# Optimization experiments

Measured on AMD Instinct MI355X. Metric: run time of the kernel, lower is better.

Reference implementation:

```python
import jax, jax.numpy as jnp
import numpy as np

NUM_HEADS = 16

def setup_inputs() -> dict:
    key = jax.random.key(0)
    k1, k2, k3 = jax.random.split(key, 3)
    B, N, C = 2, 2048, 1024
    x = jax.random.normal(k1, (B, N, C), dtype=jnp.float32)
    w_qkv = jax.random.normal(k2, (C, 3 * C), dtype=jnp.float32) * (C ** -0.5)
    w_proj = jax.random.normal(k3, (C, C), dtype=jnp.float32) * (C ** -0.5)
    b_proj = jnp.zeros((C,), dtype=jnp.float32)
    return {"x": x, "w_qkv": w_qkv, "w_proj": w_proj, "b_proj": b_proj}

def reference(x, w_qkv, w_proj, b_proj):
    B, N, C = x.shape
    H = NUM_HEADS
    D = C // H
    scale = D ** -0.5
    qkv = (x @ w_qkv).reshape(B, N, 3, H, D).transpose(2, 0, 3, 1, 4)  # [3,B,H,N,D]
    q, k, v = qkv[0], qkv[1], qkv[2]
    attn = jnp.einsum("bhnd,bhmd->bhnm", q, k) * scale  # [B,H,N,N]
    attn = jax.nn.softmax(attn, axis=-1)
    out = jnp.einsum("bhnm,bhmd->bhnd", attn, v)  # [B,H,N,D]
    out = out.transpose(0, 2, 1, 3).reshape(B, N, C)
    return out @ w_proj + b_proj
```

## Files before the change

### kernel.cpp

```cpp
#include <hip/hip_runtime.h>
#include <hip/hip_bf16.h>
#include <math.h>

#define B_SZ   2
#define N_SEQ  2048
#define C_DIM  1024
#define H_NUM  16
#define D_HEAD 64
#define M_ROWS (B_SZ * N_SEQ)
#define QKV_N  (3 * C_DIM)

typedef __attribute__((ext_vector_type(8))) short  bf16x8;
typedef __attribute__((ext_vector_type(4))) float  floatx4;

static __device__ __forceinline__ unsigned short f2bf(float x) {
    unsigned int u = __float_as_uint(x);
    u = (u + 0x7FFFu + ((u >> 16) & 1u)) >> 16;
    return (unsigned short)u;
}
static __device__ __forceinline__ unsigned int f2bf_hi(float x) {
    unsigned int u = __float_as_uint(x);
    return u + 0x7FFFu + ((u >> 16) & 1u);
}
#if __has_builtin(__builtin_amdgcn_cvt_pk_bf16_f32)
typedef __bf16 bf16_2 __attribute__((ext_vector_type(2)));
static __device__ __forceinline__ unsigned int pkbf(float a, float b) {
    union { bf16_2 v; unsigned int u; } c;
    c.v = __builtin_amdgcn_cvt_pk_bf16_f32(a, b);
    return c.u;
}
#else
static __device__ __forceinline__ unsigned int pkbf(float a, float b) {
    return __builtin_amdgcn_perm(f2bf_hi(b), f2bf_hi(a), 0x07060302u);
}
#endif

#if __has_builtin(__builtin_amdgcn_exp2f)
#define EXP2F(x) __builtin_amdgcn_exp2f(x)
#else
#define EXP2F(x) exp2f(x)
#endif

#define GLP(p) ((const __attribute__((address_space(1))) void*)(p))
#define LDP(p) ((__attribute__((address_space(3))) void*)(p))

#define CEXP 0.18033688011112042f

__global__ __launch_bounds__(256)
void prep_fused(const float* __restrict__ x,      unsigned short* __restrict__ xb,
                const float* __restrict__ w_qkv,  unsigned short* __restrict__ wqkvT,
                const float* __restrict__ w_proj, unsigned short* __restrict__ wprojT)
{
    __shared__ unsigned short t[64][72];
    const int bid = blockIdx.x;
    const int tid = threadIdx.x;

    if (bid < 4096) {
        const int i = bid * 256 + tid;
        float4 v = ((const float4*)x)[i];
        ushort4 p;
        p.x = f2bf(v.x); p.y = f2bf(v.y); p.z = f2bf(v.z); p.w = f2bf(v.w);
        ((ushort4*)xb)[i] = p;
        return;
    }

    const float* W;
    unsigned short* WT;
    int N, tt;
    if (bid < 4096 + 768) { W = w_qkv;  WT = wqkvT;  N = QKV_N; tt = bid - 4096; }
    else                  { W = w_proj; WT = wprojT; N = C_DIM; tt = bid - 4864; }
    const int ntiles = N / 64;
    const int n0 = (tt % ntiles) * 64;
    const int k0 = (tt / ntiles) * 64;
    const int K  = C_DIM;

    const int tc = tid & 15;
    const int tr = tid >> 4;
    #pragma unroll
    for (int p = 0; p < 4; ++p) {
        const int r = tr + p * 16;
        float4 v = *(const float4*)&W[(size_t)(k0 + r) * N + n0 + tc * 4];
        ushort4 pk;
        pk.x = f2bf(v.x); pk.y = f2bf(v.y); pk.z = f2bf(v.z); pk.w = f2bf(v.w);
        *(ushort4*)&t[r][tc * 4] = pk;
    }
    __syncthreads();

    const int n  = tid >> 2;
    const int c0 = (tid & 3) * 16;
    unsigned short tmp[16];
    #pragma unroll
    for (int i = 0; i < 16; ++i) tmp[i] = t[c0 + i][n];
    *(uint4*)&WT[(size_t)(n0 + n) * K + k0 + c0]     = *(uint4*)&tmp[0];
    *(uint4*)&WT[(size_t)(n0 + n) * K + k0 + c0 + 8] = *(uint4*)&tmp[8];
}

__global__ __launch_bounds__(256)
void gemm_qkv(const unsigned short* __restrict__ A,
              const unsigned short* __restrict__ BT,
              unsigned short* __restrict__ qbuf,
              unsigned short* __restrict__ kbuf,
              unsigned short* __restrict__ vbuf)
{
    const int K = C_DIM;
    __shared__ unsigned short As[128 * 64];
    __shared__ unsigned short Bs[128 * 64];

    const int tid  = threadIdx.x;
    const int lane = tid & 63;
    const int wave = tid >> 6;
    const int l15  = lane & 15;
    const int lq   = lane >> 4;
    const int e7   = l15 & 7;
    const int wm   = (wave & 1) * 64;
    const int wn   = (wave >> 1) * 64;

    const int bid = blockIdx.x;
    const int xcd = bid & 7;
    const int j   = bid >> 3;
    const int bm  = (j / 3) * 128;
    const int bn  = ((j % 3) * 8 + xcd) * 128;

    const int srow = tid >> 3;
    const int gso  = ((tid & 7) ^ (srow & 7)) * 8;

    const unsigned short* ga = A  + (size_t)(bm + srow) * K + gso;
    const unsigned short* gb = BT + (size_t)(bn + srow) * K + gso;

    floatx4 acc[4][4];
    #pragma unroll
    for (int i = 0; i < 4; ++i)
        #pragma unroll
        for (int jj = 0; jj < 4; ++jj) acc[i][jj] = (floatx4){0.f, 0.f, 0.f, 0.f};

    for (int kt = 0; kt < K; kt += 64) {
        #pragma unroll
        for (int i = 0; i < 4; ++i) {
            __builtin_amdgcn_global_load_lds(GLP(ga + (size_t)i * 32 * K + kt),
                                             LDP(&As[i * 2048 + tid * 8]), 16, 0, 0);
            __builtin_amdgcn_global_load_lds(GLP(gb + (size_t)i * 32 * K + kt),
                                             LDP(&Bs[i * 2048 + tid * 8]), 16, 0, 0);
        }
        __syncthreads();

        bf16x8 af[2][4], bfr[2][4];
        #pragma unroll
        for (int t = 0; t < 4; ++t) {
            #pragma unroll
            for (int kc = 0; kc < 2; ++kc) {
                af[kc][t]  = *(const bf16x8*)&As[(wm + t * 16 + l15) * 64
                                                 + (((kc * 4 + lq) ^ e7) * 8)];
                bfr[kc][t] = *(const bf16x8*)&Bs[(wn + t * 16 + l15) * 64
                                                 + (((kc * 4 + lq) ^ e7) * 8)];
            }
        }
        #pragma unroll
        for (int kc = 0; kc < 2; ++kc)
            #pragma unroll
            for (int mt = 0; mt < 4; ++mt)
                #pragma unroll
                for (int nt = 0; nt < 4; ++nt)
                    acc[mt][nt] = __builtin_amdgcn_mfma_f32_16x16x32_bf16(
                        af[kc][mt], bfr[kc][nt], acc[mt][nt], 0, 0, 0);
        __syncthreads();
    }

    #pragma unroll
    for (int nt = 0; nt < 4; ++nt) {
        const int col  = bn + wn + nt * 16 + l15;
        const int reg3 = col >> 10;
        const int h    = (col >> 6) & 15;
        const int d    = col & 63;
        const float sc4 = (reg3 == 0) ? CEXP : 1.0f;
        #pragma unroll
        for (int mt = 0; mt < 4; ++mt) {
            const int row = bm + wm + mt * 16 + lq * 4;
            const int b   = row >> 11;
            const int n   = row & 2047;
            if (reg3 < 2) {
                unsigned short* dst = (reg3 ? kbuf : qbuf)
                    + ((size_t)(b * H_NUM + h) * N_SEQ + n) * D_HEAD + d;
                #pragma unroll
                for (int r = 0; r < 4; ++r)
                    dst[(size_t)r * D_HEAD] = f2bf(acc[mt][nt][r] * sc4);
            } else {
                const int a  = n & 63;
                const int fk = (a & 0x20) | ((a & 0x0C) << 1) | ((a & 0x10) >> 2);
                unsigned short* dst = vbuf
                    + ((size_t)(b * H_NUM + h) * D_HEAD + d) * N_SEQ + (n & ~63) + fk;
                ushort4 pk;
                pk.x = f2bf(acc[mt][nt][0]); pk.y = f2bf(acc[mt][nt][1]);
                pk.z = f2bf(acc[mt][nt][2]); pk.w = f2bf(acc[mt][nt][3]);
                *(ushort4*)dst = pk;
            }
        }
    }
}

__global__ __launch_bounds__(512, 4)
void attn_mfma(const unsigned short* __restrict__ qbuf,
               const unsigned short* __restrict__ kbuf,
               const unsigned short* __restrict__ vbuf,
               unsigned short* __restrict__ attnb)
{
    __shared__ unsigned short KsS[2][2][64 * 64];
    __shared__ unsigned short VtS[2][2][64 * 64];

    const int tid  = threadIdx.x;
    const int lane = tid & 63;
    const int wave = tid >> 6;
    const int grp  = wave >> 2;
    const int wrow = wave & 3;
    const int l15  = lane & 15;
    const int lq   = lane >> 4;
    const int e    = l15 & 7;

    const int bid  = blockIdx.x;
    const int bh   = (bid & 7) * 4 + (bid >> 7);
    const int qblk = (bid >> 3) & 15;
    const int b    = bh >> 4;
    const int h    = bh & 15;
    const int q0   = qblk * 128 + wrow * 32;

    const unsigned short* khead = kbuf + (size_t)bh * N_SEQ * D_HEAD;
    const unsigned short* vhead = vbuf + (size_t)bh * D_HEAD * N_SEQ;

    bf16x8 qf[2][2];
    #pragma unroll
    for (int qb = 0; qb < 2; ++qb) {
        const unsigned short* qrow = qbuf
            + ((size_t)bh * N_SEQ + q0 + qb * 16 + l15) * D_HEAD + lq * 8;
        qf[0][qb] = *(const bf16x8*)qrow;
        qf[1][qb] = *(const bf16x8*)(qrow + 32);
    }

    floatx4 acc[4][2];
    #pragma unroll
    for (int dc = 0; dc < 4; ++dc)
        #pragma unroll
        for (int qb = 0; qb < 2; ++qb) acc[dc][qb] = (floatx4){0.f, 0.f, 0.f, 0.f};
    float lsum[2] = {0.f, 0.f};

    const int srow = tid >> 3;
    const int gso  = ((tid & 7) ^ (srow & 7)) * 8;

    #pragma unroll
    for (int i = 0; i < 2; ++i) {
        __builtin_amdgcn_global_load_lds(GLP(khead + (size_t)(i * 64 + srow) * 64 + gso),
                                         LDP(&KsS[0][i][tid * 8]), 16, 0, 0);
        __builtin_amdgcn_global_load_lds(GLP(vhead + (size_t)srow * N_SEQ + i * 64 + gso),
                                         LDP(&VtS[0][i][tid * 8]), 16, 0, 0);
    }

    for (int s = 0; s < N_SEQ / 128; ++s) {
        const int cur = s & 1;
        __syncthreads();

        if (s + 1 < N_SEQ / 128) {
            const int m1 = (s + 1) * 128;
            const int nx = cur ^ 1;
            #pragma unroll
            for (int i = 0; i < 2; ++i) {
                __builtin_amdgcn_global_load_lds(
                    GLP(khead + (size_t)(m1 + i * 64 + srow) * 64 + gso),
                    LDP(&KsS[nx][i][tid * 8]), 16, 0, 0);
                __builtin_amdgcn_global_load_lds(
                    GLP(vhead + (size_t)srow * N_SEQ + m1 + i * 64 + gso),
                    LDP(&VtS[nx][i][tid * 8]), 16, 0, 0);
            }
        }

        const unsigned short* Ksc = &KsS[cur][grp][0];
        const unsigned short* Vtc = &VtS[cur][grp][0];

        floatx4 st[4][2];
        #pragma unroll
        for (int t = 0; t < 4; ++t) {
            bf16x8 k0 = *(const bf16x8*)&Ksc[(t * 16 + l15) * 64 + ((lq ^ e) * 8)];
            bf16x8 k1 = *(const bf16x8*)&Ksc[(t * 16 + l15) * 64 + (((4 + lq) ^ e) * 8)];
            #pragma unroll
            for (int qb = 0; qb < 2; ++qb) {
                floatx4 sv = (floatx4){-8.f, -8.f, -8.f, -8.f};
                sv = __builtin_amdgcn_mfma_f32_16x16x32_bf16(k0, qf[0][qb], sv, 0, 0, 0);
                sv = __builtin_amdgcn_mfma_f32_16x16x32_bf16(k1, qf[1][qb], sv, 0, 0, 0);
                st[t][qb] = sv;
            }
        }

        bf16x8 pf[2][2];
        #pragma unroll
        for (int qb = 0; qb < 2; ++qb) {
            unsigned int pk[8];
            float la = 0.f;
            #pragma unroll
            for (int t = 0; t < 4; ++t) {
                float p0 = EXP2F(st[t][qb][0]);
                float p1 = EXP2F(st[t][qb][1]);
                float p2 = EXP2F(st[t][qb][2]);
                float p3 = EXP2F(st[t][qb][3]);
                la += (p0 + p1) + (p2 + p3);
                pk[t * 2]     = pkbf(p0, p1);
                pk[t * 2 + 1] = pkbf(p2, p3);
            }
            lsum[qb] += la;
            union { uint4 u; bf16x8 v; } c0, c1;
            c0.u = make_uint4(pk[0], pk[1], pk[2], pk[3]);
            c1.u = make_uint4(pk[4], pk[5], pk[6], pk[7]);
            pf[0][qb] = c0.v;
            pf[1][qb] = c1.v;
        }

        #pragma unroll
        for (int dc = 0; dc < 4; ++dc) {
            bf16x8 v0 = *(const bf16x8*)&Vtc[(dc * 16 + l15) * 64 + ((lq ^ e) * 8)];
            bf16x8 v1 = *(const bf16x8*)&Vtc[(dc * 16 + l15) * 64 + (((4 + lq) ^ e) * 8)];
            #pragma unroll
            for (int qb = 0; qb < 2; ++qb) {
                acc[dc][qb] = __builtin_amdgcn_mfma_f32_16x16x32_bf16(
                    v0, pf[0][qb], acc[dc][qb], 0, 0, 0);
                acc[dc][qb] = __builtin_amdgcn_mfma_f32_16x16x32_bf16(
                    v1, pf[1][qb], acc[dc][qb], 0, 0, 0);
            }
        }
    }

    __syncthreads();
    float* smA = (float*)&KsS[0][0][0];
    float* smL = (float*)&VtS[0][0][0];
    const int li = wrow * 64 + lane;
    if (grp) {
        float* p = smA + li * 32;
        #pragma unroll
        for (int dc = 0; dc < 4; ++dc)
            #pragma unroll
            for (int qb = 0; qb < 2; ++qb)
                #pragma unroll
                for (int r = 0; r < 4; ++r)
                    p[(dc * 8 + qb * 4 + r) ^ (lane & 31)] = acc[dc][qb][r];
        smL[li * 2]     = lsum[0];
        smL[li * 2 + 1] = lsum[1];
    }
    __syncthreads();
    if (grp) return;

    {
        const float* p = smA + li * 32;
        #pragma unroll
        for (int dc = 0; dc < 4; ++dc)
            #pragma unroll
            for (int qb = 0; qb < 2; ++qb)
                #pragma unroll
                for (int r = 0; r < 4; ++r)
                    acc[dc][qb][r] += p[(dc * 8 + qb * 4 + r) ^ (lane & 31)];
        lsum[0] += smL[li * 2];
        lsum[1] += smL[li * 2 + 1];
    }

    #pragma unroll
    for (int qb = 0; qb < 2; ++qb) {
        float l = lsum[qb];
        l += __shfl_xor(l, 16, 64);
        l += __shfl_xor(l, 32, 64);
        const float inv = 1.f / l;
        const int q = q0 + qb * 16 + l15;
        unsigned short* orow = attnb + ((size_t)b * N_SEQ + q) * C_DIM + h * D_HEAD;
        #pragma unroll
        for (int dc = 0; dc < 4; ++dc) {
            ushort4 pkk;
            pkk.x = f2bf(acc[dc][qb][0] * inv);
            pkk.y = f2bf(acc[dc][qb][1] * inv);
            pkk.z = f2bf(acc[dc][qb][2] * inv);
            pkk.w = f2bf(acc[dc][qb][3] * inv);
            *(ushort4*)&orow[dc * 16 + lq * 4] = pkk;
        }
    }
}

__global__ __launch_bounds__(256)
void gemm_bt(const unsigned short* __restrict__ A,
             const unsigned short* __restrict__ BT,
             const float* __restrict__ bias,
             float* __restrict__ Cm,
             int M, int N, int K)
{
    __shared__ unsigned short As[128 * 64];
    __shared__ unsigned short Bs[64 * 64];

    const int tid  = threadIdx.x;
    const int lane = tid & 63;
    const int wave = tid >> 6;
    const int l15  = lane & 15;
    const int lq   = lane >> 4;
    const int e7   = l15 & 7;
    const int wm   = (wave & 1) * 64;
    const int wn   = (wave >> 1) * 32;

    const int bid = blockIdx.x;
    const int xcd = bid & 7;
    const int j   = bid >> 3;
    const int bm  = (j >> 1) * 128;
    const int bn  = ((j & 1) * 8 + xcd) * 64;

    const int srow = tid >> 3;
    const int gso  = ((tid & 7) ^ (srow & 7)) * 8;

    const unsigned short* ga = A  + (size_t)(bm + srow) * K + gso;
    const unsigned short* gb = BT + (size_t)(bn + srow) * K + gso;

    floatx4 acc[4][2];
    #pragma unroll
    for (int i = 0; i < 4; ++i)
        #pragma unroll
        for (int jj = 0; jj < 2; ++jj) acc[i][jj] = (floatx4){0.f, 0.f, 0.f, 0.f};

    for (int kt = 0; kt < K; kt += 64) {
        #pragma unroll
        for (int i = 0; i < 4; ++i)
            __builtin_amdgcn_global_load_lds(GLP(ga + (size_t)i * 32 * K + kt),
                                             LDP(&As[i * 2048 + tid * 8]), 16, 0, 0);
        #pragma unroll
        for (int i = 0; i < 2; ++i)
            __builtin_amdgcn_global_load_lds(GLP(gb + (size_t)i * 32 * K + kt),
                                             LDP(&Bs[i * 2048 + tid * 8]), 16, 0, 0);
        __syncthreads();

        bf16x8 af[2][4], bfr[2][2];
        #pragma unroll
        for (int t = 0; t < 4; ++t)
            #pragma unroll
            for (int kc = 0; kc < 2; ++kc)
                af[kc][t] = *(const bf16x8*)&As[(wm + t * 16 + l15) * 64
                                                + (((kc * 4 + lq) ^ e7) * 8)];
        #pragma unroll
        for (int t = 0; t < 2; ++t)
            #pragma unroll
            for (int kc = 0; kc < 2; ++kc)
                bfr[kc][t] = *(const bf16x8*)&Bs[(wn + t * 16 + l15) * 64
                                                 + (((kc * 4 + lq) ^ e7) * 8)];
        #pragma unroll
        for (int kc = 0; kc < 2; ++kc)
            #pragma unroll
            for (int mt = 0; mt < 4; ++mt)
                #pragma unroll
                for (int nt = 0; nt < 2; ++nt)
                    acc[mt][nt] = __builtin_amdgcn_mfma_f32_16x16x32_bf16(
                        af[kc][mt], bfr[kc][nt], acc[mt][nt], 0, 0, 0);
        __syncthreads();
    }

    float bv[2];
    #pragma unroll
    for (int nt = 0; nt < 2; ++nt) bv[nt] = bias[bn + wn + nt * 16 + l15];
    #pragma unroll
    for (int mt = 0; mt < 4; ++mt) {
        const int row = bm + wm + mt * 16 + lq * 4;
        #pragma unroll
        for (int nt = 0; nt < 2; ++nt) {
            const int col = bn + wn + nt * 16 + l15;
            #pragma unroll
            for (int r = 0; r < 4; ++r)
                Cm[(size_t)(row + r) * N + col] = acc[mt][nt][r] + bv[nt];
        }
    }
}

extern "C" void kernel_launch(void* const* d_in, const int* in_sizes, int n_in,
                              void* d_out, int out_size, void* d_ws, size_t ws_size,
                              hipStream_t stream)
{
    const float* x      = (const float*)d_in[0];
    const float* w_qkv  = (const float*)d_in[1];
    const float* w_proj = (const float*)d_in[2];
    const float* b_proj = (const float*)d_in[3];
    float*       out    = (float*)d_out;

    unsigned short* xb     = (unsigned short*)d_ws;
    unsigned short* wqkvT  = xb     + (size_t)M_ROWS * C_DIM;
    unsigned short* wprojT = wqkvT  + (size_t)QKV_N * C_DIM;
    unsigned short* qbuf   = wprojT + (size_t)C_DIM * C_DIM;
    unsigned short* kbuf   = qbuf   + (size_t)M_ROWS * C_DIM;
    unsigned short* vbuf   = kbuf   + (size_t)M_ROWS * C_DIM;
    unsigned short* attnb  = vbuf   + (size_t)M_ROWS * C_DIM;

    prep_fused<<<4096 + 768 + 256, 256, 0, stream>>>(x, xb, w_qkv, wqkvT, w_proj, wprojT);

    gemm_qkv<<<768, 256, 0, stream>>>(xb, wqkvT, qbuf, kbuf, vbuf);

    attn_mfma<<<512, 512, 0, stream>>>(qbuf, kbuf, vbuf, attnb);

    gemm_bt<<<512, 256, 0, stream>>>(attnb, wprojT, b_proj, out, M_ROWS, C_DIM, C_DIM);
}
```

Before: 185.2 us.

## Double-buffer QKV GEMM with 256x256 tiles and prefetch pipeline

Rewrites the QKV projection GEMM to use 256x256 block tiles with 512 threads (8 waves, 2x4 layout) and double-buffered dynamic LDS (128 KB). Global-to-LDS loads for stage t+2 are issued while MFMAs run on the current stage, using explicit vmcnt/lgkmcnt waits and barriers. Each wave's M half is split so the second half of the A fragments loads during the first MFMA batch, and s_setprio raises wave priority around the MFMA bursts. The aim is to hide global load latency and raise operand reuse. In exchange the grid drops to 192 blocks, fewer than the CU count, and the large LDS footprint limits occupancy to one block per CU.

```diff
diff --git a/kernel.cpp b/kernel.cpp
--- a/kernel.cpp
+++ b/kernel.cpp
@@ -95,31 +95,31 @@
     *(uint4*)&WT[(size_t)(n0 + n) * K + k0 + c0 + 8] = *(uint4*)&tmp[8];
 }
 
-__global__ __launch_bounds__(256)
+__global__ __launch_bounds__(512, 2)
 void gemm_qkv(const unsigned short* __restrict__ A,
               const unsigned short* __restrict__ BT,
               unsigned short* __restrict__ qbuf,
               unsigned short* __restrict__ kbuf,
               unsigned short* __restrict__ vbuf)
 {
+    extern __shared__ unsigned short lds2[];
+    unsigned short* AsB = lds2;
+    unsigned short* BsB = lds2 + 32768;
+
     const int K = C_DIM;
-    __shared__ unsigned short As[128 * 64];
-    __shared__ unsigned short Bs[128 * 64];
-
     const int tid  = threadIdx.x;
     const int lane = tid & 63;
     const int wave = tid >> 6;
+    const int wm2  = wave >> 2;
+    const int wn4  = wave & 3;
     const int l15  = lane & 15;
     const int lq   = lane >> 4;
     const int e7   = l15 & 7;
-    const int wm   = (wave & 1) * 64;
-    const int wn   = (wave >> 1) * 64;
 
     const int bid = blockIdx.x;
-    const int xcd = bid & 7;
-    const int j   = bid >> 3;
-    const int bm  = (j / 3) * 128;
-    const int bn  = ((j % 3) * 8 + xcd) * 128;
+    const int g   = (bid & 7) * 24 + (bid >> 3);
+    const int bm  = (g & 15) * 256;
+    const int bn  = (g >> 4) * 256;
 
     const int srow = tid >> 3;
     const int gso  = ((tid & 7) ^ (srow & 7)) * 8;
@@ -127,33 +127,50 @@
     const unsigned short* ga = A  + (size_t)(bm + srow) * K + gso;
     const unsigned short* gb = BT + (size_t)(bn + srow) * K + gso;
 
-    floatx4 acc[4][4];
-    #pragma unroll
-    for (int i = 0; i < 4; ++i)
-        #pragma unroll
-        for (int jj = 0; jj < 4; ++jj) acc[i][jj] = (floatx4){0.f, 0.f, 0.f, 0.f};
-
-    for (int kt = 0; kt < K; kt += 64) {
-        #pragma unroll
-        for (int i = 0; i < 4; ++i) {
-            __builtin_amdgcn_global_load_lds(GLP(ga + (size_t)i * 32 * K + kt),
-                                             LDP(&As[i * 2048 + tid * 8]), 16, 0, 0);
-            __builtin_amdgcn_global_load_lds(GLP(gb + (size_t)i * 32 * K + kt),
-                                             LDP(&Bs[i * 2048 + tid * 8]), 16, 0, 0);
-        }
-        __syncthreads();
-
-        bf16x8 af[2][4], bfr[2][4];
-        #pragma unroll
-        for (int t = 0; t < 4; ++t) {
-            #pragma unroll
-            for (int kc = 0; kc < 2; ++kc) {
-                af[kc][t]  = *(const bf16x8*)&As[(wm + t * 16 + l15) * 64
-                                                 + (((kc * 4 + lq) ^ e7) * 8)];
-                bfr[kc][t] = *(const bf16x8*)&Bs[(wn + t * 16 + l15) * 64
-                                                 + (((kc * 4 + lq) ^ e7) * 8)];
-            }
-        }
+    floatx4 acc[8][4];
+    #pragma unroll
+    for (int i = 0; i < 8; ++i)
+        #pragma unroll
+        for (int j = 0; j < 4; ++j) acc[i][j] = (floatx4){0.f, 0.f, 0.f, 0.f};
+
+#define QKV_STAGE(t_, buf_)                                                    \
+    {                                                                          \
+        unsigned short* Ad_ = AsB + (buf_) * 16384;                            \
+        unsigned short* Bd_ = BsB + (buf_) * 16384;                            \
+        _Pragma("unroll")                                                      \
+        for (int i_ = 0; i_ < 4; ++i_) {                                       \
+            __builtin_amdgcn_global_load_lds(                                  \
+                GLP(ga + (size_t)i_ * 64 * K + (t_) * 64),                     \
+                LDP(Ad_ + i_ * 4096 + tid * 8), 16, 0, 0);                     \
+            __builtin_amdgcn_global_load_lds(                                  \
+                GLP(gb + (size_t)i_ * 64 * K + (t_) * 64),                     \
+                LDP(Bd_ + i_ * 4096 + tid * 8), 16, 0, 0);                     \
+        }                                                                      \
+    }
+
+    QKV_STAGE(0, 0);
+    QKV_STAGE(1, 1);
+    asm volatile("s_waitcnt vmcnt(8)\ns_barrier" ::: "memory");
+
+    for (int t = 0; t < 16; ++t) {
+        const int cur = t & 1;
+        const unsigned short* Ac = AsB + cur * 16384;
+        const unsigned short* Bc = BsB + cur * 16384;
+
+        bf16x8 afl[2][4], bfr[2][4];
+        #pragma unroll
+        for (int kc = 0; kc < 2; ++kc) {
+            #pragma unroll
+            for (int mt = 0; mt < 4; ++mt)
+                afl[kc][mt] = *(const bf16x8*)&Ac[(wm2 * 128 + mt * 16 + l15) * 64
+                                                  + (((kc * 4 + lq) ^ e7) * 8)];
+            #pragma unroll
+            for (int nt = 0; nt < 4; ++nt)
+                bfr[kc][nt] = *(const bf16x8*)&Bc[(wn4 * 64 + nt * 16 + l15) * 64
+                                                  + (((kc * 4 + lq) ^ e7) * 8)];
+        }
+
+        __builtin_amdgcn_s_setprio(1);
         #pragma unroll
         for (int kc = 0; kc < 2; ++kc)
             #pragma unroll
@@ -161,20 +178,47 @@
                 #pragma unroll
                 for (int nt = 0; nt < 4; ++nt)
                     acc[mt][nt] = __builtin_amdgcn_mfma_f32_16x16x32_bf16(
-                        af[kc][mt], bfr[kc][nt], acc[mt][nt], 0, 0, 0);
-        __syncthreads();
-    }
+                        afl[kc][mt], bfr[kc][nt], acc[mt][nt], 0, 0, 0);
+        __builtin_amdgcn_s_setprio(0);
+
+        bf16x8 afh[2][4];
+        #pragma unroll
+        for (int kc = 0; kc < 2; ++kc)
+            #pragma unroll
+            for (int mt = 0; mt < 4; ++mt)
+                afh[kc][mt] = *(const bf16x8*)&Ac[(wm2 * 128 + 64 + mt * 16 + l15) * 64
+                                                  + (((kc * 4 + lq) ^ e7) * 8)];
+
+        asm volatile("s_waitcnt lgkmcnt(0)\ns_barrier" ::: "memory");
+
+        if (t < 14) QKV_STAGE(t + 2, cur);
+
+        __builtin_amdgcn_s_setprio(1);
+        #pragma unroll
+        for (int kc = 0; kc < 2; ++kc)
+            #pragma unroll
+            for (int mt = 0; mt < 4; ++mt)
+                #pragma unroll
+                for (int nt = 0; nt < 4; ++nt)
+                    acc[4 + mt][nt] = __builtin_amdgcn_mfma_f32_16x16x32_bf16(
+                        afh[kc][mt], bfr[kc][nt], acc[4 + mt][nt], 0, 0, 0);
+        __builtin_amdgcn_s_setprio(0);
+
+        if (t < 14)       asm volatile("s_waitcnt vmcnt(8)\ns_barrier" ::: "memory");
+        else if (t == 14) asm volatile("s_waitcnt vmcnt(0)\ns_barrier" ::: "memory");
+    }
+#undef QKV_STAGE
 
     #pragma unroll
     for (int nt = 0; nt < 4; ++nt) {
-        const int col  = bn + wn + nt * 16 + l15;
+        const int col  = bn + wn4 * 64 + nt * 16 + l15;
         const int reg3 = col >> 10;
         const int h    = (col >> 6) & 15;
         const int d    = col & 63;
         const float sc4 = (reg3 == 0) ? CEXP : 1.0f;
         #pragma unroll
-        for (int mt = 0; mt < 4; ++mt) {
-            const int row = bm + wm + mt * 16 + lq * 4;
+        for (int mt = 0; mt < 8; ++mt) {
+            const int row = bm + wm2 * 128 + mt * 16 + lq * 4;
             const int b   = row >> 11;
             const int n   = row & 2047;
             if (reg3 < 2) {
@@ -484,7 +528,7 @@
 
     prep_fused<<<4096 + 768 + 256, 256, 0, stream>>>(x, xb, w_qkv, wqkvT, w_proj, wprojT);
 
-    gemm_qkv<<<768, 256, 0, stream>>>(xb, wqkvT, qbuf, kbuf, vbuf);
+    gemm_qkv<<<192, 512, 131072, stream>>>(xb, wqkvT, qbuf, kbuf, vbuf);
 
     attn_mfma<<<512, 512, 0, stream>>>(qbuf, kbuf, vbuf, attnb);
 
```

Result: faster. 181.2 us (-2.2%).
